# Optimization experiments

Measured on AMD Instinct MI355X. Metric: run time of the kernel, lower is better.

Reference implementation:

```python
import jax, jax.numpy as jnp
import numpy as np

E, D_MODEL, D_HIDDEN, N_TOKENS = 8, 1024, 4096, 16384


def setup_inputs() -> dict:
    key = jax.random.key(0)
    ks = jax.random.split(key, 6)
    inp = {
        "hidden_states": jax.random.normal(ks[0], (N_TOKENS, D_MODEL), jnp.float32),
        # tokens are pre-sorted by expert; equal-sized groups of N_TOKENS // E
        "fwd_expert_count": jnp.full((E,), N_TOKENS // E, dtype=jnp.int32),
        # weights stored [E, d_in, d_out] (math-equivalent transpose of torch's [E, out, in])
        "w_gelu": jax.random.normal(ks[1], (E, D_MODEL, D_HIDDEN), jnp.float32) * 0.02,
        "w_lin": jax.random.normal(ks[2], (E, D_MODEL, D_HIDDEN), jnp.float32) * 0.02,
        "b_lin": jax.random.normal(ks[3], (E, D_HIDDEN), jnp.float32) * 0.02,
        "w_o": jax.random.normal(ks[4], (E, D_HIDDEN, D_MODEL), jnp.float32) * 0.02,
        "b_o": jax.random.normal(ks[5], (E, D_MODEL), jnp.float32) * 0.02,
    }
    return inp


def reference(hidden_states, fwd_expert_count, w_gelu, w_lin, b_lin, w_o, b_o):
    # Grouped GEMM MoE expert FFN with gated GELU (T5DenseGatedActDense per expert).
    # setup_inputs uses equal group sizes, so the grouped GEMM is expressed as a
    # batched einsum over [E, capacity, d] blocks (tokens are sorted by expert).
    e, d_model, d_hidden = w_gelu.shape
    n = hidden_states.shape[0]
    cap = n // e  # per-expert token count (== fwd_expert_count[i])
    x = hidden_states.reshape(e, cap, d_model)
    # gate branch: no bias (FMoELinear bias=False), gelu_new (tanh approx)
    hidden_gelu = jax.nn.gelu(jnp.einsum('ecd,edh->ech', x, w_gelu), approximate=True)
    # linear branch: bias=True
    hidden_linear = jnp.einsum('ecd,edh->ech', x, w_lin) + b_lin[:, None, :]
    h = hidden_gelu * hidden_linear  # dropout is identity at inference
    out = jnp.einsum('ech,ehd->ecd', h, w_o) + b_o[:, None, :]
    return out.reshape(n, d_model)
```

## Files before the change

kernel.cpp:

```cpp
#include <hip/hip_runtime.h>

#define EXP 8
#define DM 1024
#define DH 4096
#define NT 16384

typedef __attribute__((ext_vector_type(8))) short bf16x8;
typedef __attribute__((ext_vector_type(4))) float f32x4;

static __device__ __forceinline__ unsigned short f2bf(float f) {
  unsigned int u = __float_as_uint(f);
  u = u + 0x7FFFu + ((u >> 16) & 1u);
  return (unsigned short)(u >> 16);
}

static __device__ __forceinline__ void gload_lds16(const void* g, void* l) {
  __builtin_amdgcn_global_load_lds((const __attribute__((address_space(1))) void*)g,
                                   (__attribute__((address_space(3))) void*)l, 16, 0, 0);
}

__global__ void cvt_bf16_k(const float* __restrict__ in, unsigned short* __restrict__ out,
                           long n4) {
  long i = (long)blockIdx.x * blockDim.x + threadIdx.x;
  const long stride = (long)gridDim.x * blockDim.x;
  for (; i < n4; i += stride) {
    const float4 v = ((const float4*)in)[i];
    ushort4 o;
    o.x = f2bf(v.x); o.y = f2bf(v.y); o.z = f2bf(v.z); o.w = f2bf(v.w);
    ((ushort4*)out)[i] = o;
  }
}

__global__ void transpose_cvt64(const float* __restrict__ src0,
                                unsigned short* __restrict__ dst0, int K, int N) {
  __shared__ float tile[64][65];
  const int t = threadIdx.x;
  const int tx = t & 15, ty = t >> 4;
  const int n0 = blockIdx.x * 64, k0 = blockIdx.y * 64;
  const int z = blockIdx.z;
  const float* src = src0 + (size_t)z * K * N;
  unsigned short* dst = dst0 + (size_t)z * K * N;
#pragma unroll
  for (int i = 0; i < 64; i += 16) {
    const float4 v = *(const float4*)&src[(size_t)(k0 + ty + i) * N + n0 + tx * 4];
    tile[ty + i][tx * 4 + 0] = v.x;
    tile[ty + i][tx * 4 + 1] = v.y;
    tile[ty + i][tx * 4 + 2] = v.z;
    tile[ty + i][tx * 4 + 3] = v.w;
  }
  __syncthreads();
#pragma unroll
  for (int i = 0; i < 64; i += 16) {
    ushort4 o;
    o.x = f2bf(tile[tx * 4 + 0][ty + i]);
    o.y = f2bf(tile[tx * 4 + 1][ty + i]);
    o.z = f2bf(tile[tx * 4 + 2][ty + i]);
    o.w = f2bf(tile[tx * 4 + 3][ty + i]);
    *(ushort4*)&dst[(size_t)(n0 + ty + i) * K + k0 + tx * 4] = o;
  }
}

__global__ void transpose_cvt64_il(const float* __restrict__ w_gelu,
                                   const float* __restrict__ w_lin,
                                   unsigned short* __restrict__ W1T) {
  __shared__ float tile[64][65];
  const int t = threadIdx.x;
  const int tx = t & 15, ty = t >> 4;
  const int n0 = blockIdx.x * 64, k0 = blockIdx.y * 64;
  const int z = blockIdx.z;
  const int gl16 = (z >> 3) * 16;
  const float* src = (z >> 3 ? w_lin : w_gelu) + (size_t)(z & 7) * DM * DH;
  unsigned short* dst = W1T + (size_t)(z & 7) * 2 * DH * DM;
#pragma unroll
  for (int i = 0; i < 64; i += 16) {
    const float4 v = *(const float4*)&src[(size_t)(k0 + ty + i) * DH + n0 + tx * 4];
    tile[ty + i][tx * 4 + 0] = v.x;
    tile[ty + i][tx * 4 + 1] = v.y;
    tile[ty + i][tx * 4 + 2] = v.z;
    tile[ty + i][tx * 4 + 3] = v.w;
  }
  __syncthreads();
#pragma unroll
  for (int i = 0; i < 64; i += 16) {
    const int n = n0 + ty + i;
    const int rowI = ((n >> 4) << 5) + (n & 15) + gl16;
    ushort4 o;
    o.x = f2bf(tile[tx * 4 + 0][ty + i]);
    o.y = f2bf(tile[tx * 4 + 1][ty + i]);
    o.z = f2bf(tile[tx * 4 + 2][ty + i]);
    o.w = f2bf(tile[tx * 4 + 3][ty + i]);
    *(ushort4*)&dst[(size_t)rowI * DM + k0 + tx * 4] = o;
  }
}


#define LDSA(row, chunk) lds[sb + (row) * 64 + ((((chunk) ^ ((row) & 7))) << 3)]
#define LDSB(row, chunk) lds[sb + 16384 + (row) * 64 + ((((chunk) ^ ((row) & 7))) << 3)]

#define RD_A(mh)                                                                   \
  _Pragma("unroll") for (int i = 0; i < 4; i++) _Pragma("unroll") for (int ks = 0; \
                                                                       ks < 2;    \
                                                                       ks++)      \
      fa[i][ks] = *(const bf16x8*)&LDSA(wr * 128 + (mh) * 64 + i * 16 + lrow, ks * 4 + khi);

#define RD_B(dst, jb)                                                              \
  _Pragma("unroll") for (int j = 0; j < 2; j++) _Pragma("unroll") for (int ks = 0; \
                                                                       ks < 2;    \
                                                                       ks++)      \
      dst[j][ks] = *(const bf16x8*)&LDSB(wc * 64 + ((jb) + j) * 16 + lrow, ks * 4 + khi);

#define MFMA16(mi, jb, fb)                                                        \
  __builtin_amdgcn_s_setprio(1);                                                  \
  _Pragma("unroll") for (int i = 0; i < 4; i++) _Pragma("unroll") for (int j = 0; \
                                                                       j < 2;    \
                                                                       j++)      \
      _Pragma("unroll") for (int ks = 0; ks < 2; ks++) acc[(mi) + i][(jb) + j] =  \
          __builtin_amdgcn_mfma_f32_16x16x32_bf16(fa[i][ks], fb[j][ks],           \
                                                  acc[(mi) + i][(jb) + j], 0, 0, 0); \
  __builtin_amdgcn_s_setprio(0);

#define BAR_FENCE()                      \
  __builtin_amdgcn_s_barrier();          \
  asm volatile("" ::: "memory");

#define PIPE_LOOP(KT)                                                   \
  STAGE_A(0, 0); STAGE_A(0, 1);                                         \
  STAGE_B(0, 0); STAGE_B(0, 1);                                         \
  STAGE_B(1, 0); STAGE_B(1, 1);                                         \
  asm volatile("s_waitcnt vmcnt(4)" ::: "memory");                      \
  BAR_FENCE();                                                          \
  for (int T = 0; T < (KT); ++T) {                                      \
    const int sb = (T & 1) * 32768;                                     \
    bf16x8 fa[4][2], fb01[2][2], fb23[2][2];                            \
    RD_A(0);                                                            \
    RD_B(fb01, 0);                                                      \
    if (T + 1 < (KT)) STAGE_A(T + 1, 0);                                \
    __builtin_amdgcn_s_barrier();                                       \
    MFMA16(0, 0, fb01);                                                 \
    BAR_FENCE();                                                        \
    RD_B(fb23, 2);                                                      \
    if (T + 1 < (KT)) STAGE_A(T + 1, 1);                                \
    __builtin_amdgcn_s_barrier();                                       \
    MFMA16(0, 2, fb23);                                                 \
    BAR_FENCE();                                                        \
    RD_A(1);                                                            \
    if (T + 2 < (KT)) STAGE_B(T + 2, 0);                                \
    __builtin_amdgcn_s_barrier();                                       \
    MFMA16(4, 2, fb23);                                                 \
    BAR_FENCE();                                                        \
    if (T + 2 < (KT)) STAGE_B(T + 2, 1);                                \
    __builtin_amdgcn_s_barrier();                                       \
    MFMA16(4, 0, fb01);                                                 \
    if (T < (KT)-2)        asm volatile("s_waitcnt vmcnt(4)" ::: "memory"); \
    else if (T == (KT)-2)  asm volatile("s_waitcnt vmcnt(0)" ::: "memory"); \
    BAR_FENCE();                                                        \
  }

__global__ __launch_bounds__(512, 1) void gemm1(
    const unsigned short* __restrict__ Xb,
    const unsigned short* __restrict__ W1T,
    const float* __restrict__ b_lin,
    unsigned short* __restrict__ Hb) {
  __shared__ unsigned short lds[65536];

  const int t = threadIdx.x;
  const int nblk = blockIdx.x, mblk = blockIdx.y;
  const int e = mblk >> 3;
  const int m0 = mblk * 256, n0 = nblk * 256;

  const int lane = t & 63, wave = t >> 6;
  const int wr = wave >> 2, wc = wave & 3;
  const int lrow = lane & 15, khi = lane >> 4;

  const int presw = (((t & 7) ^ ((t >> 3) & 7)) << 3);
  const unsigned short* gAsrc = Xb + (size_t)(m0 + (t >> 3)) * DM + presw;
  const unsigned short* gBsrc = W1T + ((size_t)e * 2 * DH + n0 + (t >> 3)) * DM + presw;

  auto STAGE_A = [&](int kt, int half) {
    unsigned short* d = &lds[(kt & 1) * 32768 + half * 8192 + t * 8];
    const unsigned short* s = gAsrc + (size_t)(half * 128) * DM + kt * 64;
    gload_lds16(s, d);
    gload_lds16(s + (size_t)64 * DM, d + 4096);
  };
  auto STAGE_B = [&](int kt, int half) {
    unsigned short* d = &lds[(kt & 1) * 32768 + 16384 + half * 8192 + t * 8];
    const unsigned short* s = gBsrc + (size_t)(half * 128) * DM + kt * 64;
    gload_lds16(s, d);
    gload_lds16(s + (size_t)64 * DM, d + 4096);
  };

  f32x4 acc[8][4];
#pragma unroll
  for (int m = 0; m < 8; m++)
#pragma unroll
    for (int j = 0; j < 4; j++) acc[m][j] = 0.0f;

  PIPE_LOOP(DM / 64);

#pragma unroll
  for (int m = 0; m < 8; m++) {
    const int rowbase = m0 + wr * 128 + (m >> 2) * 64 + (m & 3) * 16 + khi * 4;
#pragma unroll
    for (int p = 0; p < 2; p++) {
      const int hcol = nblk * 128 + (2 * wc + p) * 16 + lrow;
      const float bias = b_lin[(size_t)e * DH + hcol];
#pragma unroll
      for (int r = 0; r < 4; r++) {
        const float g = acc[m][2 * p][r];
        const float li = acc[m][2 * p + 1][r] + bias;
        const float u = 0.7978845608028654f * (g + 0.044715f * g * g * g);
        const float th = 1.0f - 2.0f / (1.0f + __expf(2.0f * u));
        const float h = 0.5f * g * (1.0f + th) * li;
        Hb[(size_t)(rowbase + r) * DH + hcol] = f2bf(h);
      }
    }
  }
}

__global__ __launch_bounds__(512, 1) void gemm2(
    const unsigned short* __restrict__ Hb,
    const unsigned short* __restrict__ WoT,
    const float* __restrict__ b_o,
    float* __restrict__ out) {
  __shared__ unsigned short lds[65536];

  const int t = threadIdx.x;
  const int nblk = blockIdx.x, mblk = blockIdx.y;
  const int e = mblk >> 3;
  const int m0 = mblk * 256, n0 = nblk * 256;

  const int lane = t & 63, wave = t >> 6;
  const int wr = wave >> 2, wc = wave & 3;
  const int lrow = lane & 15, khi = lane >> 4;

  const int presw = (((t & 7) ^ ((t >> 3) & 7)) << 3);
  const unsigned short* gAsrc = Hb + (size_t)(m0 + (t >> 3)) * DH + presw;
  const unsigned short* gBsrc = WoT + ((size_t)e * DM + n0 + (t >> 3)) * DH + presw;

  auto STAGE_A = [&](int kt, int half) {
    unsigned short* d = &lds[(kt & 1) * 32768 + half * 8192 + t * 8];
    const unsigned short* s = gAsrc + (size_t)(half * 128) * DH + kt * 64;
    gload_lds16(s, d);
    gload_lds16(s + (size_t)64 * DH, d + 4096);
  };
  auto STAGE_B = [&](int kt, int half) {
    unsigned short* d = &lds[(kt & 1) * 32768 + 16384 + half * 8192 + t * 8];
    const unsigned short* s = gBsrc + (size_t)(half * 128) * DH + kt * 64;
    gload_lds16(s, d);
    gload_lds16(s + (size_t)64 * DH, d + 4096);
  };

  f32x4 acc[8][4];
#pragma unroll
  for (int m = 0; m < 8; m++)
#pragma unroll
    for (int j = 0; j < 4; j++) acc[m][j] = 0.0f;

  PIPE_LOOP(DH / 64);

  const float* bop = b_o + (size_t)e * DM;
#pragma unroll
  for (int m = 0; m < 8; m++) {
    const int rowbase = m0 + wr * 128 + (m >> 2) * 64 + (m & 3) * 16 + khi * 4;
#pragma unroll
    for (int j = 0; j < 4; j++) {
      const int gcol = n0 + wc * 64 + j * 16 + lrow;
      const float bias = bop[gcol];
#pragma unroll
      for (int r = 0; r < 4; r++)
        out[(size_t)(rowbase + r) * DM + gcol] = acc[m][j][r] + bias;
    }
  }
}

extern "C" void kernel_launch(void* const* d_in, const int* in_sizes, int n_in,
                              void* d_out, int out_size, void* d_ws, size_t ws_size,
                              hipStream_t stream) {
  const float* hs = (const float*)d_in[0];
  const float* w_gelu = (const float*)d_in[2];
  const float* w_lin = (const float*)d_in[3];
  const float* b_lin = (const float*)d_in[4];
  const float* w_o = (const float*)d_in[5];
  const float* b_o = (const float*)d_in[6];
  float* outp = (float*)d_out;

  unsigned short* Xb = (unsigned short*)d_ws;
  unsigned short* W1T = Xb + (size_t)NT * DM;
  unsigned short* WoT = W1T + (size_t)EXP * 2 * DH * DM;
  unsigned short* Hb = WoT + (size_t)EXP * DH * DM;

  cvt_bf16_k<<<dim3(2048), dim3(256), 0, stream>>>(hs, Xb, (long)NT * DM / 4);
  transpose_cvt64_il<<<dim3(DH / 64, DM / 64, 16), dim3(256), 0, stream>>>(
      w_gelu, w_lin, W1T);
  transpose_cvt64<<<dim3(DM / 64, DH / 64, 8), dim3(256), 0, stream>>>(w_o, WoT, DH, DM);

  gemm1<<<dim3(2 * DH / 256, NT / 256), dim3(512), 0, stream>>>(Xb, W1T, b_lin, Hb);
  gemm2<<<dim3(DM / 256, NT / 256), dim3(512), 0, stream>>>(Hb, WoT, b_o, outp);
}
```

Before: 559.3 us.

## Retile gemm1 to 256x128 tiles with 4 waves, K-step 32, two blocks per CU

```diff
diff --git a/kernel.cpp b/kernel.cpp
--- a/kernel.cpp
+++ b/kernel.cpp
@@ -94,6 +94,137 @@
 }
 
 
+#define G1_LDSA(row, c) lds[sb + (row) * 32 + ((((c) ^ ((row) & 3))) << 3)]
+#define G1_LDSB(row, c) lds[sb + 8192 + (row) * 32 + ((((c) ^ ((row) & 3))) << 3)]
+
+__global__ __launch_bounds__(256, 2) void gemm1(
+    const unsigned short* __restrict__ Xb,
+    const unsigned short* __restrict__ W1T,
+    const float* __restrict__ b_lin,
+    unsigned short* __restrict__ Hb) {
+  __shared__ unsigned short lds[2 * 12288];
+
+  const int t = threadIdx.x;
+  const int nblk = blockIdx.x, mblk = blockIdx.y;
+  const int e = mblk >> 3;
+  const int m0 = mblk * 256;
+  const int lane = t & 63, wave = t >> 6;
+  const int wr = wave >> 1, wc = wave & 1;
+  const int lrow = lane & 15, khi = lane >> 4;
+
+  const int presw = (((t & 3) ^ ((t >> 2) & 3)) << 3);
+  const unsigned short* gAsrc = Xb + (size_t)(m0 + (t >> 2)) * DM + presw;
+  const unsigned short* gBsrc =
+      W1T + ((size_t)e * 2 * DH + nblk * 128 + (t >> 2)) * DM + presw;
+
+  const int KT = DM / 32;
+
+  auto STAGE_A = [&](int kt, int u) {
+    unsigned short* d = &lds[(kt & 1) * 12288 + u * 2048 + t * 8];
+    gload_lds16(gAsrc + (size_t)(u * 64) * DM + kt * 32, d);
+  };
+  auto STAGE_B = [&](int kt, int u) {
+    unsigned short* d = &lds[(kt & 1) * 12288 + 8192 + u * 2048 + t * 8];
+    gload_lds16(gBsrc + (size_t)(u * 64) * DM + kt * 32, d);
+  };
+
+  f32x4 acc[8][4];
+#pragma unroll
+  for (int m = 0; m < 8; m++)
+#pragma unroll
+    for (int j = 0; j < 4; j++) acc[m][j] = 0.0f;
+
+  STAGE_A(0, 0); STAGE_A(0, 1); STAGE_A(0, 2); STAGE_A(0, 3);
+  STAGE_B(0, 0); STAGE_B(0, 1);
+  STAGE_B(1, 0); STAGE_B(1, 1);
+  asm volatile("s_waitcnt vmcnt(2)" ::: "memory");
+  __builtin_amdgcn_s_barrier();
+  asm volatile("" ::: "memory");
+
+  for (int T = 0; T < KT; ++T) {
+    const int sb = (T & 1) * 12288;
+    bf16x8 fa[4], fb01[2], fb23[2];
+#pragma unroll
+    for (int i = 0; i < 4; i++)
+      fa[i] = *(const bf16x8*)&G1_LDSA(wr * 128 + i * 16 + lrow, khi);
+#pragma unroll
+    for (int j = 0; j < 2; j++)
+      fb01[j] = *(const bf16x8*)&G1_LDSB(wc * 64 + j * 16 + lrow, khi);
+    if (T + 1 < KT) { STAGE_A(T + 1, 0); STAGE_A(T + 1, 1); }
+    __builtin_amdgcn_s_barrier();
+    __builtin_amdgcn_s_setprio(1);
+#pragma unroll
+    for (int i = 0; i < 4; i++)
+#pragma unroll
+      for (int j = 0; j < 2; j++)
+        acc[i][j] = __builtin_amdgcn_mfma_f32_16x16x32_bf16(fa[i], fb01[j], acc[i][j], 0, 0, 0);
+    __builtin_amdgcn_s_setprio(0);
+    __builtin_amdgcn_s_barrier();
+    asm volatile("" ::: "memory");
+#pragma unroll
+    for (int j = 0; j < 2; j++)
+      fb23[j] = *(const bf16x8*)&G1_LDSB(wc * 64 + (2 + j) * 16 + lrow, khi);
+    if (T + 1 < KT) { STAGE_A(T + 1, 2); STAGE_A(T + 1, 3); }
+    __builtin_amdgcn_s_barrier();
+    __builtin_amdgcn_s_setprio(1);
+#pragma unroll
+    for (int i = 0; i < 4; i++)
+#pragma unroll
+      for (int j = 0; j < 2; j++)
+        acc[i][2 + j] = __builtin_amdgcn_mfma_f32_16x16x32_bf16(fa[i], fb23[j], acc[i][2 + j], 0, 0, 0);
+    __builtin_amdgcn_s_setprio(0);
+    __builtin_amdgcn_s_barrier();
+    asm volatile("" ::: "memory");
+#pragma unroll
+    for (int i = 0; i < 4; i++)
+      fa[i] = *(const bf16x8*)&G1_LDSA(wr * 128 + 64 + i * 16 + lrow, khi);
+    if (T + 2 < KT) STAGE_B(T + 2, 0);
+    __builtin_amdgcn_s_barrier();
+    __builtin_amdgcn_s_setprio(1);
+#pragma unroll
+    for (int i = 0; i < 4; i++)
+#pragma unroll
+      for (int j = 0; j < 2; j++)
+        acc[4 + i][2 + j] = __builtin_amdgcn_mfma_f32_16x16x32_bf16(fa[i], fb23[j], acc[4 + i][2 + j], 0, 0, 0);
+    __builtin_amdgcn_s_setprio(0);
+    __builtin_amdgcn_s_barrier();
+    asm volatile("" ::: "memory");
+    if (T + 2 < KT) STAGE_B(T + 2, 1);
+    __builtin_amdgcn_s_barrier();
+    __builtin_amdgcn_s_setprio(1);
+#pragma unroll
+    for (int i = 0; i < 4; i++)
+#pragma unroll
+      for (int j = 0; j < 2; j++)
+        acc[4 + i][j] = __builtin_amdgcn_mfma_f32_16x16x32_bf16(fa[i], fb01[j], acc[4 + i][j], 0, 0, 0);
+    __builtin_amdgcn_s_setprio(0);
+    if (T < KT - 2)       asm volatile("s_waitcnt vmcnt(2)" ::: "memory");
+    else if (T == KT - 2) asm volatile("s_waitcnt vmcnt(0)" ::: "memory");
+    __builtin_amdgcn_s_barrier();
+    asm volatile("" ::: "memory");
+  }
+
+#pragma unroll
+  for (int m = 0; m < 8; m++) {
+    const int rowbase = m0 + wr * 128 + (m >> 2) * 64 + (m & 3) * 16 + khi * 4;
+#pragma unroll
+    for (int p = 0; p < 2; p++) {
+      const int hcol = nblk * 64 + wc * 32 + p * 16 + lrow;
+      const float bias = b_lin[(size_t)e * DH + hcol];
+#pragma unroll
+      for (int r = 0; r < 4; r++) {
+        const float g = acc[m][2 * p][r];
+        const float li = acc[m][2 * p + 1][r] + bias;
+        const float u = 0.7978845608028654f * (g + 0.044715f * g * g * g);
+        const float th = 1.0f - 2.0f / (1.0f + __expf(2.0f * u));
+        const float h = 0.5f * g * (1.0f + th) * li;
+        Hb[(size_t)(rowbase + r) * DH + hcol] = f2bf(h);
+      }
+    }
+  }
+}
+
+
 #define LDSA(row, chunk) lds[sb + (row) * 64 + ((((chunk) ^ ((row) & 7))) << 3)]
 #define LDSB(row, chunk) lds[sb + 16384 + (row) * 64 + ((((chunk) ^ ((row) & 7))) << 3)]
 
@@ -123,100 +254,6 @@
   __builtin_amdgcn_s_barrier();          \
   asm volatile("" ::: "memory");
 
-#define PIPE_LOOP(KT)                                                   \
-  STAGE_A(0, 0); STAGE_A(0, 1);                                         \
-  STAGE_B(0, 0); STAGE_B(0, 1);                                         \
-  STAGE_B(1, 0); STAGE_B(1, 1);                                         \
-  asm volatile("s_waitcnt vmcnt(4)" ::: "memory");                      \
-  BAR_FENCE();                                                          \
-  for (int T = 0; T < (KT); ++T) {                                      \
-    const int sb = (T & 1) * 32768;                                     \
-    bf16x8 fa[4][2], fb01[2][2], fb23[2][2];                            \
-    RD_A(0);                                                            \
-    RD_B(fb01, 0);                                                      \
-    if (T + 1 < (KT)) STAGE_A(T + 1, 0);                                \
-    __builtin_amdgcn_s_barrier();                                       \
-    MFMA16(0, 0, fb01);                                                 \
-    BAR_FENCE();                                                        \
-    RD_B(fb23, 2);                                                      \
-    if (T + 1 < (KT)) STAGE_A(T + 1, 1);                                \
-    __builtin_amdgcn_s_barrier();                                       \
-    MFMA16(0, 2, fb23);                                                 \
-    BAR_FENCE();                                                        \
-    RD_A(1);                                                            \
-    if (T + 2 < (KT)) STAGE_B(T + 2, 0);                                \
-    __builtin_amdgcn_s_barrier();                                       \
-    MFMA16(4, 2, fb23);                                                 \
-    BAR_FENCE();                                                        \
-    if (T + 2 < (KT)) STAGE_B(T + 2, 1);                                \
-    __builtin_amdgcn_s_barrier();                                       \
-    MFMA16(4, 0, fb01);                                                 \
-    if (T < (KT)-2)        asm volatile("s_waitcnt vmcnt(4)" ::: "memory"); \
-    else if (T == (KT)-2)  asm volatile("s_waitcnt vmcnt(0)" ::: "memory"); \
-    BAR_FENCE();                                                        \
-  }
-
-__global__ __launch_bounds__(512, 1) void gemm1(
-    const unsigned short* __restrict__ Xb,
-    const unsigned short* __restrict__ W1T,
-    const float* __restrict__ b_lin,
-    unsigned short* __restrict__ Hb) {
-  __shared__ unsigned short lds[65536];
-
-  const int t = threadIdx.x;
-  const int nblk = blockIdx.x, mblk = blockIdx.y;
-  const int e = mblk >> 3;
-  const int m0 = mblk * 256, n0 = nblk * 256;
-
-  const int lane = t & 63, wave = t >> 6;
-  const int wr = wave >> 2, wc = wave & 3;
-  const int lrow = lane & 15, khi = lane >> 4;
-
-  const int presw = (((t & 7) ^ ((t >> 3) & 7)) << 3);
-  const unsigned short* gAsrc = Xb + (size_t)(m0 + (t >> 3)) * DM + presw;
-  const unsigned short* gBsrc = W1T + ((size_t)e * 2 * DH + n0 + (t >> 3)) * DM + presw;
-
-  auto STAGE_A = [&](int kt, int half) {
-    unsigned short* d = &lds[(kt & 1) * 32768 + half * 8192 + t * 8];
-    const unsigned short* s = gAsrc + (size_t)(half * 128) * DM + kt * 64;
-    gload_lds16(s, d);
-    gload_lds16(s + (size_t)64 * DM, d + 4096);
-  };
-  auto STAGE_B = [&](int kt, int half) {
-    unsigned short* d = &lds[(kt & 1) * 32768 + 16384 + half * 8192 + t * 8];
-    const unsigned short* s = gBsrc + (size_t)(half * 128) * DM + kt * 64;
-    gload_lds16(s, d);
-    gload_lds16(s + (size_t)64 * DM, d + 4096);
-  };
-
-  f32x4 acc[8][4];
-#pragma unroll
-  for (int m = 0; m < 8; m++)
-#pragma unroll
-    for (int j = 0; j < 4; j++) acc[m][j] = 0.0f;
-
-  PIPE_LOOP(DM / 64);
-
-#pragma unroll
-  for (int m = 0; m < 8; m++) {
-    const int rowbase = m0 + wr * 128 + (m >> 2) * 64 + (m & 3) * 16 + khi * 4;
-#pragma unroll
-    for (int p = 0; p < 2; p++) {
-      const int hcol = nblk * 128 + (2 * wc + p) * 16 + lrow;
-      const float bias = b_lin[(size_t)e * DH + hcol];
-#pragma unroll
-      for (int r = 0; r < 4; r++) {
-        const float g = acc[m][2 * p][r];
-        const float li = acc[m][2 * p + 1][r] + bias;
-        const float u = 0.7978845608028654f * (g + 0.044715f * g * g * g);
-        const float th = 1.0f - 2.0f / (1.0f + __expf(2.0f * u));
-        const float h = 0.5f * g * (1.0f + th) * li;
-        Hb[(size_t)(rowbase + r) * DH + hcol] = f2bf(h);
-      }
-    }
-  }
-}
-
 __global__ __launch_bounds__(512, 1) void gemm2(
     const unsigned short* __restrict__ Hb,
     const unsigned short* __restrict__ WoT,
@@ -236,6 +273,8 @@
   const int presw = (((t & 7) ^ ((t >> 3) & 7)) << 3);
   const unsigned short* gAsrc = Hb + (size_t)(m0 + (t >> 3)) * DH + presw;
   const unsigned short* gBsrc = WoT + ((size_t)e * DM + n0 + (t >> 3)) * DH + presw;
+
+  const int KT = DH / 64;
 
   auto STAGE_A = [&](int kt, int half) {
     unsigned short* d = &lds[(kt & 1) * 32768 + half * 8192 + t * 8];
@@ -256,7 +295,38 @@
 #pragma unroll
     for (int j = 0; j < 4; j++) acc[m][j] = 0.0f;
 
-  PIPE_LOOP(DH / 64);
+  STAGE_A(0, 0); STAGE_A(0, 1);
+  STAGE_B(0, 0); STAGE_B(0, 1);
+  STAGE_B(1, 0); STAGE_B(1, 1);
+  asm volatile("s_waitcnt vmcnt(4)" ::: "memory");
+  BAR_FENCE();
+
+  for (int T = 0; T < KT; ++T) {
+    const int sb = (T & 1) * 32768;
+    bf16x8 fa[4][2], fb01[2][2], fb23[2][2];
+    RD_A(0);
+    RD_B(fb01, 0);
+    if (T + 1 < KT) STAGE_A(T + 1, 0);
+    __builtin_amdgcn_s_barrier();
+    MFMA16(0, 0, fb01);
+    BAR_FENCE();
+    RD_B(fb23, 2);
+    if (T + 1 < KT) STAGE_A(T + 1, 1);
+    __builtin_amdgcn_s_barrier();
+    MFMA16(0, 2, fb23);
+    BAR_FENCE();
+    RD_A(1);
+    if (T + 2 < KT) STAGE_B(T + 2, 0);
+    __builtin_amdgcn_s_barrier();
+    MFMA16(4, 2, fb23);
+    BAR_FENCE();
+    if (T + 2 < KT) STAGE_B(T + 2, 1);
+    __builtin_amdgcn_s_barrier();
+    MFMA16(4, 0, fb01);
+    if (T < KT - 2)       asm volatile("s_waitcnt vmcnt(4)" ::: "memory");
+    else if (T == KT - 2) asm volatile("s_waitcnt vmcnt(0)" ::: "memory");
+    BAR_FENCE();
+  }
 
   const float* bop = b_o + (size_t)e * DM;
 #pragma unroll
@@ -294,6 +364,6 @@
       w_gelu, w_lin, W1T);
   transpose_cvt64<<<dim3(DM / 64, DH / 64, 8), dim3(256), 0, stream>>>(w_o, WoT, DH, DM);
 
-  gemm1<<<dim3(2 * DH / 256, NT / 256), dim3(512), 0, stream>>>(Xb, W1T, b_lin, Hb);
+  gemm1<<<dim3(2 * DH / 128, NT / 256), dim3(256), 0, stream>>>(Xb, W1T, b_lin, Hb);
   gemm2<<<dim3(DM / 256, NT / 256), dim3(512), 0, stream>>>(Hb, WoT, b_o, outp);
 }
```

Measured after the change: 585.9 us. 1.05x slower.
